# Optimization experiments

Hardware: AMD Instinct MI355X
Metric: run time of the kernel (lower is better)

Reference implementation:

```python
import jax, jax.numpy as jnp
import numpy as np

B, S = 64, 512
NQ, RAW, D, H, K = 10000, 256, 256, 64, 4  # vocab, raw emb, model emb, gru state, num_stages
LN_EPS = 1e-5


def setup_inputs() -> dict:
    key = jax.random.key(0)
    ks = jax.random.split(key, 30)
    def n(i, shape, s=0.02):
        return (jax.random.normal(ks[i], shape) * s).astype(jnp.float32)
    return {
        "q": jax.random.randint(ks[0], (B, S), 0, NQ, dtype=jnp.int32),
        "r": jax.random.randint(ks[1], (B, S), 0, 2, dtype=jnp.int32),
        # flattened 4-stage embedding table [NQ*4, RAW]
        "emb_table": n(2, (NQ * K, RAW)),
        # per-stage expert MLPs (weights stored as [in, out])
        "expert_w1": n(3, (K, RAW, RAW)), "expert_b1": n(4, (K, RAW)),
        "expert_w2": n(5, (K, RAW, D)),  "expert_b2": n(6, (K, D)),
        # router input adapter Linear(RAW*4 -> D)
        "adapter_w": n(7, (RAW * K, D)), "adapter_b": n(8, (D,)),
        # interaction reducer Linear(2D -> H)
        "reducer_w": n(9, (2 * D, H)), "reducer_b": n(10, (H,)),
        "start_token": jnp.zeros((1, 1, H), jnp.float32),
        # torch GRU params: [3H, in], gate order (r, z, n)
        "gru_w_ih": n(11, (3 * H, H)), "gru_w_hh": n(12, (3 * H, H)),
        "gru_b_ih": n(13, (3 * H,)),   "gru_b_hh": n(14, (3 * H,)),
        # gate Linear(D+H -> 4)
        "wgate_w": n(15, (D + H, K)), "wgate_b": n(16, (K,)),
        "ln_gamma": jnp.ones((D,), jnp.float32), "ln_beta": jnp.zeros((D,), jnp.float32),
        "resp_table": n(17, (2, D)),
        "proj_cor_w": n(18, (D, D)), "proj_cor_b": n(19, (D,)),
        "proj_inc_w": n(20, (D, D)), "proj_inc_b": n(21, (D,)),
    }


def _forward(q, r, emb_table, expert_w1, expert_b1, expert_w2, expert_b2,
             adapter_w, adapter_b, reducer_w, reducer_b, start_token,
             gru_w_ih, gru_w_hh, gru_b_ih, gru_b_hh, wgate_w, wgate_b,
             ln_gamma, ln_beta, resp_table, proj_cor_w, proj_cor_b,
             proj_inc_w, proj_inc_b):
    b, s = q.shape
    # 4-stage embedding lookup: indices q*4 + [0..3]
    stage_idx = q[..., None] * K + jnp.arange(K)          # [B,S,4]
    q_raw = emb_table[stage_idx]                          # [B,S,4,RAW]
    # smart summary (router input adapter), eval mode -> no dropout
    q_flat = q_raw.reshape(b, s, K * RAW)
    q_summary = jax.nn.relu(q_flat @ adapter_w + adapter_b)  # [B,S,D]
    r_emb = resp_table[r]                                    # [B,S,D]
    gru_in = jnp.concatenate([q_summary, r_emb], -1) @ reducer_w + reducer_b  # [B,S,H]
    start = jnp.broadcast_to(start_token, (b, 1, H))
    x = jnp.concatenate([start, gru_in[:, :-1]], axis=1)     # shifted [B,S,H]
    # GRU over time (torch gate order r,z,n)
    xg = x @ gru_w_ih.T + gru_b_ih                           # [B,S,3H]
    def step(h, xg_t):
        hg = h @ gru_w_hh.T + gru_b_hh
        xr, xz, xn = jnp.split(xg_t, 3, axis=-1)
        hr, hz, hn = jnp.split(hg, 3, axis=-1)
        rg = jax.nn.sigmoid(xr + hr)
        zg = jax.nn.sigmoid(xz + hz)
        ng = jnp.tanh(xn + rg * hn)
        h_new = (1.0 - zg) * ng + zg * h
        return h_new, h_new
    _, m = jax.lax.scan(step, jnp.zeros((b, H), x.dtype), xg.transpose(1, 0, 2))
    m_seq = m.transpose(1, 0, 2)                             # [B,S,H]
    # parallel experts (vectorized over the 4 stages)
    h1 = jax.nn.relu(jnp.einsum('bske,keh->bskh', q_raw, expert_w1) + expert_b1)
    experts = jnp.einsum('bskh,khd->bskd', h1, expert_w2) + expert_b2  # [B,S,4,D]
    # noisy routing (eval: no noise), top-1 mask, softmax gating
    logits = jnp.concatenate([q_summary, m_seq], -1) @ wgate_w + wgate_b  # [B,S,4]
    gate_probs = jax.nn.softmax(logits, axis=-1)
    top1 = jnp.argmax(logits, axis=-1)
    onehot = jax.nn.one_hot(top1, K, dtype=logits.dtype)
    masked = jnp.where(onehot > 0, logits, -jnp.inf)
    gate_w = jax.nn.softmax(masked, axis=-1)                 # one-hot for top_k=1
    combined = jnp.einsum('bskd,bsk->bsd', experts, gate_w)  # [B,S,D]
    # layer norm
    mu = combined.mean(-1, keepdims=True)
    var = combined.var(-1, keepdims=True)
    q_fused = ln_gamma * (combined - mu) * jax.lax.rsqrt(var + LN_EPS) + ln_beta
    emb_cor = q_fused @ proj_cor_w + proj_cor_b
    emb_inc = q_fused @ proj_inc_w + proj_inc_b
    rm = r[..., None].astype(q_fused.dtype)
    qa_fused = emb_cor * rm + emb_inc * (1.0 - rm)
    return q_fused, qa_fused, gate_probs


def reference(q, r, emb_table, expert_w1, expert_b1, expert_w2, expert_b2,
              adapter_w, adapter_b, reducer_w, reducer_b, start_token,
              gru_w_ih, gru_w_hh, gru_b_ih, gru_b_hh, wgate_w, wgate_b,
              ln_gamma, ln_beta, resp_table, proj_cor_w, proj_cor_b,
              proj_inc_w, proj_inc_b):
    q_fused, qa_fused, _ = _forward(q, r, emb_table, expert_w1, expert_b1,
                                    expert_w2, expert_b2, adapter_w, adapter_b,
                                    reducer_w, reducer_b, start_token,
                                    gru_w_ih, gru_w_hh, gru_b_ih, gru_b_hh,
                                    wgate_w, wgate_b, ln_gamma, ln_beta,
                                    resp_table, proj_cor_w, proj_cor_b,
                                    proj_inc_w, proj_inc_b)
    return (q_fused, qa_fused)
```

## Files before the change

kernel.cpp:

```cpp
#include <hip/hip_runtime.h>
#include <cstddef>


#define NQ 10000
#define TT 32768

typedef __attribute__((ext_vector_type(8))) short bf16x8;
typedef __attribute__((ext_vector_type(4))) float f32x4;

__device__ double g_qs  [NQ * 256];
__device__ double g_xgr [2 * 192];
__device__ float  g_xg0f[192];
__device__ float  g_xq2 [NQ * 384];
__device__ double g_lq  [NQ * 4];
__device__ float  g_m   [TT * 64];
__device__ unsigned short g_w1t  [4 * 256 * 256];
__device__ unsigned short g_w2t  [4 * 256 * 256];
__device__ unsigned short g_projt[512 * 256];
__device__ unsigned short g_qf   [NQ * 4 * 256];

__device__ __forceinline__ float bf2f(unsigned short x) {
  return __uint_as_float(((unsigned)x) << 16);
}
__device__ __forceinline__ unsigned short f2bf(float f) {
  unsigned u = __float_as_uint(f);
  u += 0x7FFFu + ((u >> 16) & 1u);
  return (unsigned short)(u >> 16);
}
__device__ __forceinline__ f32x4 mfma16(bf16x8 a, bf16x8 b, f32x4 c) {
  return __builtin_amdgcn_mfma_f32_16x16x32_bf16(a, b, c, 0, 0, 0);
}
__device__ __forceinline__ void pkfma(float2& c, float2 a, float2 b) {
  asm("v_pk_fma_f32 %0, %1, %2, %0" : "+v"(c) : "v"(a), "v"(b));
}

__device__ __forceinline__ double fexp(double x) {
  const double L2E  = 1.4426950408889634074;
  const double LN2H = 6.93147180369123816490e-01;
  const double LN2L = 1.90821492927058770002e-10;
  double n = rint(x * L2E);
  int ni = (int)n;
  double r = fma(-n, LN2H, x);
  r = fma(-n, LN2L, r);
  double p = 2.7557319223985888e-07;
  p = fma(p, r, 2.7557319223985893e-06);
  p = fma(p, r, 2.4801587301587302e-05);
  p = fma(p, r, 1.9841269841269841e-04);
  p = fma(p, r, 1.3888888888888889e-03);
  p = fma(p, r, 8.3333333333333332e-03);
  p = fma(p, r, 4.1666666666666664e-02);
  p = fma(p, r, 1.6666666666666666e-01);
  p = fma(p, r, 0.5);
  p = fma(p, r, 1.0);
  p = fma(p, r, 1.0);
  return ldexp(p, ni);
}

__device__ __forceinline__ double tpoly(double p) {
  const double p2 = p * p;
  double t = -1382.0 / 155925.0;
  t = fma(t, p2, 62.0 / 2835.0);
  t = fma(t, p2, -17.0 / 315.0);
  t = fma(t, p2, 2.0 / 15.0);
  t = fma(t, p2, -1.0 / 3.0);
  t = fma(t, p2, 1.0);
  return p * t;
}

__global__ void __launch_bounds__(256) prepqsk_kernel(
    const float* __restrict__ expert_w1, const float* __restrict__ expert_w2,
    const float* __restrict__ proj_cor_w, const float* __restrict__ proj_inc_w,
    const float* __restrict__ resp_table, const float* __restrict__ reducer_w,
    const float* __restrict__ reducer_b,  const float* __restrict__ start_token,
    const float* __restrict__ gru_w_ih,   const float* __restrict__ gru_b_ih,
    const float* __restrict__ emb, const float* __restrict__ adapter_w,
    const float* __restrict__ adapter_b)
{
  __shared__ double red2f[128];
  __shared__ __align__(16) float As[32][66];
  __shared__ __align__(16) float Bs[32][65];
  const int tid = threadIdx.x;

  if (blockIdx.x < 64) {
    if (blockIdx.x == 0) {
      if (tid < 128) {
        const int rr = tid >> 6, j = tid & 63;
        double acc = (double)reducer_b[j];
        for (int k = 0; k < 256; ++k)
          acc += (double)resp_table[rr * 256 + k] *
                 (double)reducer_w[(256 + k) * 64 + j];
        red2f[tid] = acc;
      }
      __syncthreads();
      if (tid < 192) {
        const double bih = (double)gru_b_ih[tid];
        double a0 = bih, a1 = bih, a2 = bih;
        for (int j = 0; j < 64; ++j) {
          const double w = (double)gru_w_ih[tid * 64 + j];
          a0 += red2f[j] * w;
          a1 += red2f[64 + j] * w;
          a2 += (double)start_token[j] * w;
        }
        g_xgr[tid] = a0; g_xgr[192 + tid] = a1; g_xg0f[tid] = (float)a2;
      }
    }
    const int idx0 = blockIdx.x * 256 + tid;
    const int stride = 64 * 256;
    for (int i = idx0; i < 4 * 256 * 256; i += stride) {
      const int e = i >> 16, rem = i & 65535, n = rem >> 8, k = rem & 255;
      g_w1t[i] = f2bf(expert_w1[e * 65536 + k * 256 + n]);
      g_w2t[i] = f2bf(expert_w2[e * 65536 + k * 256 + n]);
    }
    for (int i = idx0; i < 512 * 256; i += stride) {
      const int n = i >> 8, k = i & 255;
      g_projt[i] = f2bf((n < 256) ? proj_cor_w[k * 256 + n]
                                  : proj_inc_w[k * 256 + (n - 256)]);
    }
    return;
  }

  const int bq = blockIdx.x - 64;
  const int q0 = (bq >> 2) * 64;
  const int n0 = (bq & 3) * 64;
  const int ty = tid >> 4, tx = tid & 15;

  double acc[4][4];
#pragma unroll
  for (int i = 0; i < 4; ++i)
#pragma unroll
    for (int j = 0; j < 4; ++j) acc[i][j] = 0.0;

  const int arow = tid >> 2, aks = (tid & 3) * 8;
  const int qa = min(q0 + arow, NQ - 1);
  const int bkk = tid >> 3, bns = (tid & 7) * 8;

  for (int kc = 0; kc < 1024; kc += 32) {
    f32x4 av0 = *(const f32x4*)(emb + (size_t)qa * 1024 + kc + aks);
    f32x4 av1 = *(const f32x4*)(emb + (size_t)qa * 1024 + kc + aks + 4);
    f32x4 bv0 = *(const f32x4*)(adapter_w + (size_t)(kc + bkk) * 256 + n0 + bns);
    f32x4 bv1 = *(const f32x4*)(adapter_w + (size_t)(kc + bkk) * 256 + n0 + bns + 4);
    __syncthreads();
#pragma unroll
    for (int i = 0; i < 4; ++i) {
      As[aks + i][arow] = av0[i];
      As[aks + 4 + i][arow] = av1[i];
      Bs[bkk][bns + i] = bv0[i];
      Bs[bkk][bns + 4 + i] = bv1[i];
    }
    __syncthreads();
#pragma unroll 4
    for (int kk = 0; kk < 32; ++kk) {
      const f32x4 af = *(const f32x4*)&As[kk][ty * 4];
      const f32x4 bf = *(const f32x4*)&Bs[kk][tx * 4];
      double a[4], b[4];
#pragma unroll
      for (int i = 0; i < 4; ++i) a[i] = (double)af[i];
#pragma unroll
      for (int j = 0; j < 4; ++j) b[j] = (double)bf[j];
#pragma unroll
      for (int i = 0; i < 4; ++i)
#pragma unroll
        for (int j = 0; j < 4; ++j) acc[i][j] = fma(a[i], b[j], acc[i][j]);
    }
  }
#pragma unroll
  for (int i = 0; i < 4; ++i) {
    const int qrow = q0 + ty * 4 + i;
    if (qrow < NQ) {
#pragma unroll
      for (int j = 0; j < 4; ++j) {
        const int n = n0 + tx * 4 + j;
        double v = acc[i][j] + (double)adapter_b[n];
        g_qs[(size_t)qrow * 256 + n] = v > 0.0 ? v : 0.0;
      }
    }
  }
}

__global__ void __launch_bounds__(256) smallk_kernel(
    const float* __restrict__ reducer_w, const float* __restrict__ gru_w_ih,
    const float* __restrict__ wgate_w)
{
  __shared__ float rwl[256 * 64];
  __shared__ float gwl[192 * 64];
  __shared__ float wgl[256 * 4];
  __shared__ double qsr[256];
  __shared__ double ps[4][64];
  __shared__ double gi[64];
  const int tid = threadIdx.x;

  for (int i = tid; i < 256 * 64; i += 256) rwl[i] = reducer_w[i];
  for (int i = tid; i < 192 * 64; i += 256) gwl[i] = gru_w_ih[i];
  for (int i = tid; i < 256 * 4; i += 256) wgl[i] = wgate_w[i];

  for (int g = 0; g < 8; ++g) {
    const int qq = blockIdx.x * 8 + g;
    __syncthreads();
    qsr[tid] = g_qs[(size_t)qq * 256 + tid];
    __syncthreads();
    {
      const int j = tid & 63, h = tid >> 6;
      const int k0 = h * 64;
      double a0 = 0.0, a1 = 0.0, a2 = 0.0, a3 = 0.0;
      for (int k = 0; k < 64; k += 4) {
        a0 = fma(qsr[k0 + k + 0], (double)rwl[(k0 + k + 0) * 64 + j], a0);
        a1 = fma(qsr[k0 + k + 1], (double)rwl[(k0 + k + 1) * 64 + j], a1);
        a2 = fma(qsr[k0 + k + 2], (double)rwl[(k0 + k + 2) * 64 + j], a2);
        a3 = fma(qsr[k0 + k + 3], (double)rwl[(k0 + k + 3) * 64 + j], a3);
      }
      ps[h][j] = (a0 + a1) + (a2 + a3);
    }
    __syncthreads();
    if (tid < 64) gi[tid] = (ps[0][tid] + ps[1][tid]) + (ps[2][tid] + ps[3][tid]);
    if (tid >= 64 && tid < 68) {
      const int e = tid - 64;
      double a0 = 0.0, a1 = 0.0, a2 = 0.0, a3 = 0.0;
      for (int k = 0; k < 256; k += 4) {
        a0 = fma(qsr[k + 0], (double)wgl[(k + 0) * 4 + e], a0);
        a1 = fma(qsr[k + 1], (double)wgl[(k + 1) * 4 + e], a1);
        a2 = fma(qsr[k + 2], (double)wgl[(k + 2) * 4 + e], a2);
        a3 = fma(qsr[k + 3], (double)wgl[(k + 3) * 4 + e], a3);
      }
      g_lq[(size_t)qq * 4 + e] = (a0 + a1) + (a2 + a3);
    }
    __syncthreads();
    if (tid < 192) {
      double a0 = 0.0, a1 = 0.0, a2 = 0.0, a3 = 0.0;
      for (int k = 0; k < 64; k += 4) {
        a0 = fma(gi[k + 0], (double)gwl[tid * 64 + k + 0], a0);
        a1 = fma(gi[k + 1], (double)gwl[tid * 64 + k + 1], a1);
        a2 = fma(gi[k + 2], (double)gwl[tid * 64 + k + 2], a2);
        a3 = fma(gi[k + 3], (double)gwl[tid * 64 + k + 3], a3);
      }
      const double s = (a0 + a1) + (a2 + a3);
      g_xq2[(size_t)qq * 384 + tid]       = (float)(s + g_xgr[tid]);
      g_xq2[(size_t)qq * 384 + 192 + tid] = (float)(s + g_xgr[192 + tid]);
    }
  }
}

__global__ void __attribute__((amdgpu_waves_per_eu(1, 1)))
__launch_bounds__(128, 1) gruE_kernel(
    const int* __restrict__ q, const int* __restrict__ r,
    const float* __restrict__ whh, const float* __restrict__ bhh,
    const float* __restrict__ emb,
    const float* __restrict__ b1, const float* __restrict__ b2,
    const float* __restrict__ lng, const float* __restrict__ lnb)
{
  __shared__ __align__(16) float HF[2][68];
  __shared__ __align__(16) unsigned short QR[32 * 264];
  __shared__ __align__(16) unsigned short H1[32 * 264];
  __shared__ __align__(16) unsigned short EO[32 * 264];
  const int tid = threadIdx.x;

  if (blockIdx.x < 64) {
    const int b = blockIdx.x;
    const int wv = tid >> 6;
    const int l = tid & 63;
    const int p = l >> 1;
    const int half = l & 1;
    const int j = wv * 32 + p;
    const int k0 = half * 32;

    float2 Wr[16], Wz[16], Wn[16];
#pragma unroll
    for (int i = 0; i < 16; ++i) {
      Wr[i] = *(const float2*)(whh + (size_t)(0 * 64 + j) * 64 + k0 + 2 * i);
      Wz[i] = *(const float2*)(whh + (size_t)(1 * 64 + j) * 64 + k0 + 2 * i);
      Wn[i] = *(const float2*)(whh + (size_t)(2 * 64 + j) * 64 + k0 + 2 * i);
    }
#pragma unroll
    for (int i = 0; i < 16; ++i) {
      asm volatile("" : "+v"(Wr[i]));
      asm volatile("" : "+v"(Wz[i]));
      asm volatile("" : "+v"(Wn[i]));
    }
    const double br = (double)bhh[j];
    const double bz = (double)bhh[64 + j];
    const double bn = (double)bhh[128 + j];

    float cx0 = g_xg0f[j], cx1 = g_xg0f[64 + j], cx2 = g_xg0f[128 + j];
    int qA = q[b * 512], rA = r[b * 512];

    const int jpad = j + ((j >> 5) << 2);
    if (tid < 64) {
      const int tp = tid + ((tid >> 5) << 2);
      HF[0][tp] = 0.f;
    }
    double hd = 0.0;
    asm volatile("s_waitcnt lgkmcnt(0)\n\ts_barrier" ::: "memory");

    for (int t = 0; t < 512; ++t) {
      float nx0 = 0.f, nx1 = 0.f, nx2 = 0.f;
      int qB = qA, rB = rA;
      if (t < 511) {
        const size_t base = (size_t)(qA * 2 + rA) * 192 + j;
        nx0 = g_xq2[base];
        nx1 = g_xq2[base + 64];
        nx2 = g_xq2[base + 128];
        const int tk = min(t + 1, 510);
        qB = q[b * 512 + tk];
        rB = r[b * 512 + tk];
      }

      float2 ar = {0.f, 0.f}, az = {0.f, 0.f}, an = {0.f, 0.f};
      {
        const float4* hp = (const float4*)&HF[t & 1][half * 36];
#pragma unroll
        for (int g = 0; g < 8; ++g) {
          const float4 t4 = hp[g];
          const float2 hA = make_float2(t4.x, t4.y);
          const float2 hB = make_float2(t4.z, t4.w);
          pkfma(ar, Wr[2 * g], hA); pkfma(ar, Wr[2 * g + 1], hB);
          pkfma(az, Wz[2 * g], hA); pkfma(az, Wz[2 * g + 1], hB);
          pkfma(an, Wn[2 * g], hA); pkfma(an, Wn[2 * g + 1], hB);
        }
      }
      const float srh = ar.x + ar.y;
      const float szh = az.x + az.y;
      const float snh = an.x + an.y;
      const float sro = __shfl_xor(srh, 1);
      const float szo = __shfl_xor(szh, 1);
      const float sno = __shfl_xor(snh, 1);
      const double hr = br + ((double)srh + (double)sro);
      const double hz = bz + ((double)szh + (double)szo);
      const double hn = bn + ((double)snh + (double)sno);
      const double pr = (double)cx0 + hr, pz = (double)cx1 + hz;
      const double xn = (double)cx2;
      double rg = fma(0.5, tpoly(0.5 * pr), 0.5);
      double zg = fma(0.5, tpoly(0.5 * pz), 0.5);
      double pre = fma(rg, hn, xn);
      double ng = tpoly(pre);
      const bool bad = (fabs(pr) > 0.5) | (fabs(pz) > 0.5) | (fabs(pre) > 0.25);
      if (bad) {
        rg = 1.0 / (1.0 + fexp(-pr));
        zg = 1.0 / (1.0 + fexp(-pz));
        pre = fma(rg, hn, xn);
        ng = 1.0 - 2.0 / (fexp(pre + pre) + 1.0);
      }
      const double hnew = fma(zg, hd - ng, ng);
      hd = hnew;
      const float hnf = (float)hnew;
      if (half == 0) {
        HF[(t & 1) ^ 1][jpad] = hnf;
        g_m[((size_t)b * 512 + t) * 64 + j] = hnf;
      }
      asm volatile("s_waitcnt lgkmcnt(0)\n\ts_barrier" ::: "memory");

      cx0 = nx0; cx1 = nx1; cx2 = nx2;
      qA = qB; rA = rB;
    }
    return;
  }

  const int bx = blockIdx.x - 64;
  const int e  = bx & 3;
  const int t0 = (bx >> 2) * 32;
  const int w = tid >> 6;
  const int lane = tid & 63;
  const int l15 = lane & 15;
  const int quad = lane >> 4;

  for (int c = 0; c < 16; ++c) {
    const int idx = c * 128 + tid;
    const int row = idx >> 6, col4 = idx & 63;
    const int qv = min(t0 + row, NQ - 1);
    f32x4 v = *(const f32x4*)(emb + (size_t)qv * 1024 + e * 256 + col4 * 4);
    unsigned a = ((unsigned)f2bf(v[1]) << 16) | f2bf(v[0]);
    unsigned bb = ((unsigned)f2bf(v[3]) << 16) | f2bf(v[2]);
    *(uint2*)&QR[row * 264 + col4 * 4] = make_uint2(a, bb);
  }
  __syncthreads();

  const f32x4 z4 = {0.f, 0.f, 0.f, 0.f};
  const int n0 = w * 128;

  f32x4 acc[2][8];
#pragma unroll
  for (int a = 0; a < 2; ++a)
#pragma unroll
    for (int bq = 0; bq < 8; ++bq) acc[a][bq] = z4;
#pragma unroll
  for (int ks = 0; ks < 8; ++ks) {
    const int koff = ks * 32 + quad * 8;
    bf16x8 a0 = *(const bf16x8*)&QR[l15 * 264 + koff];
    bf16x8 a1 = *(const bf16x8*)&QR[(16 + l15) * 264 + koff];
#pragma unroll
    for (int nt = 0; nt < 8; ++nt) {
      bf16x8 bbv = *(const bf16x8*)(g_w1t + (size_t)e * 65536 +
                                    (size_t)(n0 + nt * 16 + l15) * 256 + koff);
      acc[0][nt] = mfma16(a0, bbv, acc[0][nt]);
      acc[1][nt] = mfma16(a1, bbv, acc[1][nt]);
    }
  }
#pragma unroll
  for (int nt = 0; nt < 8; ++nt) {
    const int n = n0 + nt * 16 + l15;
    const float b1v = b1[e * 256 + n];
#pragma unroll
    for (int mt = 0; mt < 2; ++mt)
#pragma unroll
      for (int rg = 0; rg < 4; ++rg) {
        const int m = mt * 16 + quad * 4 + rg;
        H1[m * 264 + n] = f2bf(fmaxf(acc[mt][nt][rg] + b1v, 0.f));
      }
  }
  __syncthreads();

  f32x4 acc2[2][8];
#pragma unroll
  for (int a = 0; a < 2; ++a)
#pragma unroll
    for (int bq = 0; bq < 8; ++bq) acc2[a][bq] = z4;
#pragma unroll
  for (int ks = 0; ks < 8; ++ks) {
    const int koff = ks * 32 + quad * 8;
    bf16x8 a0 = *(const bf16x8*)&H1[l15 * 264 + koff];
    bf16x8 a1 = *(const bf16x8*)&H1[(16 + l15) * 264 + koff];
#pragma unroll
    for (int nt = 0; nt < 8; ++nt) {
      bf16x8 bbv = *(const bf16x8*)(g_w2t + (size_t)e * 65536 +
                                    (size_t)(n0 + nt * 16 + l15) * 256 + koff);
      acc2[0][nt] = mfma16(a0, bbv, acc2[0][nt]);
      acc2[1][nt] = mfma16(a1, bbv, acc2[1][nt]);
    }
  }
#pragma unroll
  for (int nt = 0; nt < 8; ++nt) {
    const int n = n0 + nt * 16 + l15;
    const float b2v = b2[e * 256 + n];
#pragma unroll
    for (int mt = 0; mt < 2; ++mt)
#pragma unroll
      for (int rg = 0; rg < 4; ++rg) {
        const int m = mt * 16 + quad * 4 + rg;
        EO[m * 264 + n] = f2bf(acc2[mt][nt][rg] + b2v);
      }
  }
  __syncthreads();

  {
    const int m = tid >> 2;
    const int sub = tid & 3;
    float sx = 0.f, sxx = 0.f;
#pragma unroll
    for (int i = 0; i < 8; ++i) {
      bf16x8 v = *(const bf16x8*)&EO[m * 264 + sub * 64 + i * 8];
#pragma unroll
      for (int c = 0; c < 8; ++c) {
        const float f = bf2f((unsigned short)v[c]);
        sx += f; sxx += f * f;
      }
    }
    sx += __shfl_xor(sx, 1); sxx += __shfl_xor(sxx, 1);
    sx += __shfl_xor(sx, 2); sxx += __shfl_xor(sxx, 2);
    const float mu = sx * (1.f / 256.f);
    const float var = sxx * (1.f / 256.f) - mu * mu;
    const float inv = 1.f / sqrtf(var + 1e-5f);
    if (t0 + m < NQ) {
      const size_t base = ((size_t)(t0 + m) * 4 + e) * 256;
#pragma unroll
      for (int i = 0; i < 8; ++i) {
        const int dbase = sub * 64 + i * 8;
        bf16x8 v = *(const bf16x8*)&EO[m * 264 + dbase];
        bf16x8 ov;
#pragma unroll
        for (int c = 0; c < 8; ++c) {
          const int d = dbase + c;
          const float f = bf2f((unsigned short)v[c]);
          ov[c] = (short)f2bf(lng[d] * (f - mu) * inv + lnb[d]);
        }
        *(bf16x8*)(g_qf + base + dbase) = ov;
      }
    }
  }
}

__global__ void __launch_bounds__(128) kernelF(
    const int* __restrict__ q, const int* __restrict__ r,
    const float* __restrict__ wgate_w, const float* __restrict__ wgate_b,
    const float* __restrict__ pcb, const float* __restrict__ pib,
    float* __restrict__ out)
{
  __shared__ __align__(16) unsigned short QF[32 * 264];
  __shared__ double w2d[256];
  __shared__ int rv_l[32];
  const int tid = threadIdx.x;
  const int t0 = blockIdx.x * 32;
  const int w = tid >> 6;
  const int lane = tid & 63;
  const int l15 = lane & 15;
  const int quad = lane >> 4;
  if (tid < 32) rv_l[tid] = r[t0 + tid];
  w2d[tid] = (double)wgate_w[1024 + tid];
  w2d[128 + tid] = (double)wgate_w[1152 + tid];
  __syncthreads();

  int bi;
  {
    const int tok = tid >> 2;
    const int e = tid & 3;
    const int t = t0 + tok;
    const int qv = q[t];
    double le = g_lq[(size_t)qv * 4 + e] + (double)wgate_b[e];
    const f32x4* mr4 = (const f32x4*)(g_m + (size_t)t * 64);
#pragma unroll 4
    for (int jj = 0; jj < 16; ++jj) {
      const f32x4 mv4 = mr4[jj];
#pragma unroll
      for (int c = 0; c < 4; ++c)
        le = fma((double)mv4[c], w2d[(jj * 4 + c) * 4 + e], le);
    }
    double v = le; bi = e;
    {
      const double vo = __shfl_xor(v, 1);
      const int bo = __shfl_xor(bi, 1);
      const bool ilow = (e & 1) == 0;
      const double vl = ilow ? v : vo, vh = ilow ? vo : v;
      const int bl = ilow ? bi : bo, bh = ilow ? bo : bi;
      if (vh > vl) { v = vh; bi = bh; } else { v = vl; bi = bl; }
    }
    {
      const double vo = __shfl_xor(v, 2);
      const int bo = __shfl_xor(bi, 2);
      const bool ilow = (e & 2) == 0;
      const double vl = ilow ? v : vo, vh = ilow ? vo : v;
      const int bl = ilow ? bi : bo, bh = ilow ? bo : bi;
      if (vh > vl) { v = vh; bi = bh; } else { v = vl; bi = bl; }
    }
  }

  {
    const int m = tid >> 2;
    const size_t row = ((size_t)q[t0 + m] * 4 + bi) * 256;
#pragma unroll
    for (int i = 0; i < 8; ++i) {
      const int dbase = (tid & 3) * 64 + i * 8;
      bf16x8 v = *(const bf16x8*)(g_qf + row + dbase);
      *(bf16x8*)&QF[m * 264 + dbase] = v;
      f32x4 f0, f1;
#pragma unroll
      for (int c = 0; c < 4; ++c) f0[c] = bf2f((unsigned short)v[c]);
#pragma unroll
      for (int c = 0; c < 4; ++c) f1[c] = bf2f((unsigned short)v[4 + c]);
      *(f32x4*)(out + (size_t)(t0 + m) * 256 + dbase) = f0;
      *(f32x4*)(out + (size_t)(t0 + m) * 256 + dbase + 4) = f1;
    }
  }
  __syncthreads();

  const f32x4 z4 = {0.f, 0.f, 0.f, 0.f};
  const int n0 = w * 128;
  for (int ph = 0; ph < 2; ++ph) {
    f32x4 acc[2][8];
#pragma unroll
    for (int a = 0; a < 2; ++a)
#pragma unroll
      for (int bq = 0; bq < 8; ++bq) acc[a][bq] = z4;
#pragma unroll
    for (int ks = 0; ks < 8; ++ks) {
      const int koff = ks * 32 + quad * 8;
      bf16x8 a0 = *(const bf16x8*)&QF[l15 * 264 + koff];
      bf16x8 a1 = *(const bf16x8*)&QF[(16 + l15) * 264 + koff];
#pragma unroll
      for (int nt = 0; nt < 8; ++nt) {
        bf16x8 bbv = *(const bf16x8*)(g_projt +
            (size_t)(ph * 256 + n0 + nt * 16 + l15) * 256 + koff);
        acc[0][nt] = mfma16(a0, bbv, acc[0][nt]);
        acc[1][nt] = mfma16(a1, bbv, acc[1][nt]);
      }
    }
    const float* pbb = ph ? pib : pcb;
    const int want = ph ? 0 : 1;
#pragma unroll
    for (int nt = 0; nt < 8; ++nt) {
      const int n = n0 + nt * 16 + l15;
      const float pbv = pbb[n];
#pragma unroll
      for (int mt = 0; mt < 2; ++mt)
#pragma unroll
        for (int rg = 0; rg < 4; ++rg) {
          const int m = mt * 16 + quad * 4 + rg;
          if (rv_l[m] == want)
            out[(size_t)TT * 256 + (size_t)(t0 + m) * 256 + n] =
                acc[mt][nt][rg] + pbv;
        }
    }
  }
}

extern "C" void kernel_launch(void* const* d_in, const int* in_sizes, int n_in,
                              void* d_out, int out_size, void* d_ws, size_t ws_size,
                              hipStream_t stream)
{
  const int*   q   = (const int*)d_in[0];
  const int*   r   = (const int*)d_in[1];
  const float* emb = (const float*)d_in[2];
  const float* ew1 = (const float*)d_in[3];
  const float* eb1 = (const float*)d_in[4];
  const float* ew2 = (const float*)d_in[5];
  const float* eb2 = (const float*)d_in[6];
  const float* aw  = (const float*)d_in[7];
  const float* ab  = (const float*)d_in[8];
  const float* rw  = (const float*)d_in[9];
  const float* rb  = (const float*)d_in[10];
  const float* st  = (const float*)d_in[11];
  const float* wih = (const float*)d_in[12];
  const float* whh = (const float*)d_in[13];
  const float* bih = (const float*)d_in[14];
  const float* bhh = (const float*)d_in[15];
  const float* wgw = (const float*)d_in[16];
  const float* wgb = (const float*)d_in[17];
  const float* lng = (const float*)d_in[18];
  const float* lnb = (const float*)d_in[19];
  const float* resp= (const float*)d_in[20];
  const float* pcw = (const float*)d_in[21];
  const float* pcb = (const float*)d_in[22];
  const float* piw = (const float*)d_in[23];
  const float* pib = (const float*)d_in[24];
  float* out = (float*)d_out;
  (void)bih; (void)in_sizes; (void)n_in; (void)d_ws; (void)ws_size; (void)out_size;

  prepqsk_kernel<<<692, 256, 0, stream>>>(ew1, ew2, pcw, piw, resp, rw, rb, st,
                                          wih, bih, emb, aw, ab);
  smallk_kernel<<<1250, 256, 0, stream>>>(rw, wih, wgw);
  gruE_kernel<<<64 + 313 * 4, 128, 0, stream>>>(q, r, whh, bhh,
                                                emb, eb1, eb2, lng, lnb);
  kernelF<<<1024, 128, 0, stream>>>(q, r, wgw, wgb, pcb, pib, out);
}
```

Baseline: 909.1 us.

## Drop LDS weight staging in smallk and relayout adapter GEMM A-tile

smallk_kernel no longer copies reducer_w, gru_w_ih and wgate_w into about 130KB of LDS per block. It now launches one block per vocabulary entry and reads the weights straight from global memory, relying on L2 to hold them. This removes a large per-block prologue and raises occupancy, at the cost of repeated global and L2 weight reads. Separately, the adapter GEMM A tile is stored row-major with a padded stride of 33, so the transposed scattered stores go away. The compute loop then reads it with scalar LDS loads instead of vector f32x4 loads.

New measurement: 764.7 us. 15.9% less time.

```diff
diff --git a/kernel.cpp b/kernel.cpp
--- a/kernel.cpp
+++ b/kernel.cpp
@@ -77,7 +77,7 @@
     const float* __restrict__ adapter_b)
 {
   __shared__ double red2f[128];
-  __shared__ __align__(16) float As[32][66];
+  __shared__ __align__(16) float As[64][33];
   __shared__ __align__(16) float Bs[32][65];
   const int tid = threadIdx.x;
 
@@ -141,22 +141,17 @@
     f32x4 bv1 = *(const f32x4*)(adapter_w + (size_t)(kc + bkk) * 256 + n0 + bns + 4);
     __syncthreads();
 #pragma unroll
-    for (int i = 0; i < 4; ++i) {
-      As[aks + i][arow] = av0[i];
-      As[aks + 4 + i][arow] = av1[i];
-      Bs[bkk][bns + i] = bv0[i];
-      Bs[bkk][bns + 4 + i] = bv1[i];
-    }
+    for (int i = 0; i < 4; ++i) { As[arow][aks + i] = av0[i]; As[arow][aks + 4 + i] = av1[i]; }
+#pragma unroll
+    for (int i = 0; i < 4; ++i) { Bs[bkk][bns + i] = bv0[i]; Bs[bkk][bns + 4 + i] = bv1[i]; }
     __syncthreads();
 #pragma unroll 4
     for (int kk = 0; kk < 32; ++kk) {
-      const f32x4 af = *(const f32x4*)&As[kk][ty * 4];
-      const f32x4 bf = *(const f32x4*)&Bs[kk][tx * 4];
       double a[4], b[4];
 #pragma unroll
-      for (int i = 0; i < 4; ++i) a[i] = (double)af[i];
-#pragma unroll
-      for (int j = 0; j < 4; ++j) b[j] = (double)bf[j];
+      for (int i = 0; i < 4; ++i) a[i] = (double)As[ty * 4 + i][kk];
+#pragma unroll
+      for (int j = 0; j < 4; ++j) b[j] = (double)Bs[kk][tx * 4 + j];
 #pragma unroll
       for (int i = 0; i < 4; ++i)
 #pragma unroll
@@ -181,61 +176,50 @@
     const float* __restrict__ reducer_w, const float* __restrict__ gru_w_ih,
     const float* __restrict__ wgate_w)
 {
-  __shared__ float rwl[256 * 64];
-  __shared__ float gwl[192 * 64];
-  __shared__ float wgl[256 * 4];
   __shared__ double qsr[256];
   __shared__ double ps[4][64];
   __shared__ double gi[64];
   const int tid = threadIdx.x;
-
-  for (int i = tid; i < 256 * 64; i += 256) rwl[i] = reducer_w[i];
-  for (int i = tid; i < 192 * 64; i += 256) gwl[i] = gru_w_ih[i];
-  for (int i = tid; i < 256 * 4; i += 256) wgl[i] = wgate_w[i];
-
-  for (int g = 0; g < 8; ++g) {
-    const int qq = blockIdx.x * 8 + g;
-    __syncthreads();
-    qsr[tid] = g_qs[(size_t)qq * 256 + tid];
-    __syncthreads();
-    {
-      const int j = tid & 63, h = tid >> 6;
-      const int k0 = h * 64;
-      double a0 = 0.0, a1 = 0.0, a2 = 0.0, a3 = 0.0;
-      for (int k = 0; k < 64; k += 4) {
-        a0 = fma(qsr[k0 + k + 0], (double)rwl[(k0 + k + 0) * 64 + j], a0);
-        a1 = fma(qsr[k0 + k + 1], (double)rwl[(k0 + k + 1) * 64 + j], a1);
-        a2 = fma(qsr[k0 + k + 2], (double)rwl[(k0 + k + 2) * 64 + j], a2);
-        a3 = fma(qsr[k0 + k + 3], (double)rwl[(k0 + k + 3) * 64 + j], a3);
-      }
-      ps[h][j] = (a0 + a1) + (a2 + a3);
-    }
-    __syncthreads();
-    if (tid < 64) gi[tid] = (ps[0][tid] + ps[1][tid]) + (ps[2][tid] + ps[3][tid]);
-    if (tid >= 64 && tid < 68) {
-      const int e = tid - 64;
-      double a0 = 0.0, a1 = 0.0, a2 = 0.0, a3 = 0.0;
-      for (int k = 0; k < 256; k += 4) {
-        a0 = fma(qsr[k + 0], (double)wgl[(k + 0) * 4 + e], a0);
-        a1 = fma(qsr[k + 1], (double)wgl[(k + 1) * 4 + e], a1);
-        a2 = fma(qsr[k + 2], (double)wgl[(k + 2) * 4 + e], a2);
-        a3 = fma(qsr[k + 3], (double)wgl[(k + 3) * 4 + e], a3);
-      }
-      g_lq[(size_t)qq * 4 + e] = (a0 + a1) + (a2 + a3);
-    }
-    __syncthreads();
-    if (tid < 192) {
-      double a0 = 0.0, a1 = 0.0, a2 = 0.0, a3 = 0.0;
-      for (int k = 0; k < 64; k += 4) {
-        a0 = fma(gi[k + 0], (double)gwl[tid * 64 + k + 0], a0);
-        a1 = fma(gi[k + 1], (double)gwl[tid * 64 + k + 1], a1);
-        a2 = fma(gi[k + 2], (double)gwl[tid * 64 + k + 2], a2);
-        a3 = fma(gi[k + 3], (double)gwl[tid * 64 + k + 3], a3);
-      }
-      const double s = (a0 + a1) + (a2 + a3);
-      g_xq2[(size_t)qq * 384 + tid]       = (float)(s + g_xgr[tid]);
-      g_xq2[(size_t)qq * 384 + 192 + tid] = (float)(s + g_xgr[192 + tid]);
-    }
+  const int qq = blockIdx.x;
+  qsr[tid] = g_qs[(size_t)qq * 256 + tid];
+  __syncthreads();
+  {
+    const int j = tid & 63, h = tid >> 6;
+    const int k0 = h * 64;
+    double a0 = 0.0, a1 = 0.0, a2 = 0.0, a3 = 0.0;
+    for (int k = 0; k < 64; k += 4) {
+      a0 = fma(qsr[k0 + k + 0], (double)reducer_w[(k0 + k + 0) * 64 + j], a0);
+      a1 = fma(qsr[k0 + k + 1], (double)reducer_w[(k0 + k + 1) * 64 + j], a1);
+      a2 = fma(qsr[k0 + k + 2], (double)reducer_w[(k0 + k + 2) * 64 + j], a2);
+      a3 = fma(qsr[k0 + k + 3], (double)reducer_w[(k0 + k + 3) * 64 + j], a3);
+    }
+    ps[h][j] = (a0 + a1) + (a2 + a3);
+  }
+  __syncthreads();
+  if (tid < 64) gi[tid] = (ps[0][tid] + ps[1][tid]) + (ps[2][tid] + ps[3][tid]);
+  if (tid >= 64 && tid < 68) {
+    const int e = tid - 64;
+    double a0 = 0.0, a1 = 0.0, a2 = 0.0, a3 = 0.0;
+    for (int k = 0; k < 256; k += 4) {
+      a0 = fma(qsr[k + 0], (double)wgate_w[(k + 0) * 4 + e], a0);
+      a1 = fma(qsr[k + 1], (double)wgate_w[(k + 1) * 4 + e], a1);
+      a2 = fma(qsr[k + 2], (double)wgate_w[(k + 2) * 4 + e], a2);
+      a3 = fma(qsr[k + 3], (double)wgate_w[(k + 3) * 4 + e], a3);
+    }
+    g_lq[(size_t)qq * 4 + e] = (a0 + a1) + (a2 + a3);
+  }
+  __syncthreads();
+  if (tid < 192) {
+    double a0 = 0.0, a1 = 0.0, a2 = 0.0, a3 = 0.0;
+    for (int k = 0; k < 64; k += 4) {
+      a0 = fma(gi[k + 0], (double)gru_w_ih[tid * 64 + k + 0], a0);
+      a1 = fma(gi[k + 1], (double)gru_w_ih[tid * 64 + k + 1], a1);
+      a2 = fma(gi[k + 2], (double)gru_w_ih[tid * 64 + k + 2], a2);
+      a3 = fma(gi[k + 3], (double)gru_w_ih[tid * 64 + k + 3], a3);
+    }
+    const double s = (a0 + a1) + (a2 + a3);
+    g_xq2[(size_t)qq * 384 + tid]       = (float)(s + g_xgr[tid]);
+    g_xq2[(size_t)qq * 384 + 192 + tid] = (float)(s + g_xgr[192 + tid]);
   }
 }
 
@@ -623,7 +607,7 @@
 
   prepqsk_kernel<<<692, 256, 0, stream>>>(ew1, ew2, pcw, piw, resp, rw, rb, st,
                                           wih, bih, emb, aw, ab);
-  smallk_kernel<<<1250, 256, 0, stream>>>(rw, wih, wgw);
+  smallk_kernel<<<NQ, 256, 0, stream>>>(rw, wih, wgw);
   gruE_kernel<<<64 + 313 * 4, 128, 0, stream>>>(q, r, whh, bhh,
                                                 emb, eb1, eb2, lng, lnb);
   kernelF<<<1024, 128, 0, stream>>>(q, r, wgw, wgb, pcb, pib, out);
```
